# Kernel tuning notes

Hardware: AMD Instinct MI355X
Metric: run time of the kernel (lower is better)

The kernel has to match this reference:

```python
import jax, jax.numpy as jnp
import numpy as np
import math

H = 16  # n_heads


def setup_inputs() -> dict:
    key = jax.random.key(0)
    ks = jax.random.split(key, 12)
    B, S, D = 8, 1024, 1024
    inp = {
        "query": jax.random.normal(ks[0], (B, S, D), jnp.float32),
        "key_": jax.random.normal(ks[1], (B, S, D), jnp.float32),
        "value": jax.random.normal(ks[2], (B, S, D), jnp.float32),
        "mask": jnp.ones((B, S, S), jnp.int32),
        "attn_pos": jax.random.normal(ks[3], (1, H, S, S), jnp.float32),
    }
    sc = 1.0 / math.sqrt(D)
    for i, nm in enumerate(["q", "k", "v", "o"]):
        inp[f"w{nm}"] = jax.random.normal(ks[4 + i], (D, D), jnp.float32) * sc
        inp[f"b{nm}"] = jax.random.normal(ks[8 + i], (D,), jnp.float32) * 0.01
    return inp


def reference(query, key_, value, mask, attn_pos, wq, bq, wk, bk, wv, bv, wo, bo):
    B, S, D = query.shape
    dk = D // H

    def proj(x, w, b):  # [B,S,D] -> [B,H,S,dk]
        return (x @ w.T + b).reshape(B, S, H, dk).transpose(0, 2, 1, 3)

    q = proj(query, wq, bq)
    k = proj(key_, wk, bk)
    v = proj(value, wv, bv)

    # attn_pos branch: scale by sqrt(2*d_k), add positional bias
    scores = jnp.einsum("bhqd,bhkd->bhqk", q, k) / math.sqrt(2 * dk) + attn_pos
    scores = jnp.where(mask[:, None] == 0, -1e9, scores)
    p = jax.nn.softmax(scores, axis=-1)  # dropout inactive (eval)
    x = jnp.einsum("bhqk,bhkd->bhqd", p, v)
    x = x.transpose(0, 2, 1, 3).reshape(B, S, D)
    x = x @ wo.T + bo          # linears[-1] applied once...
    return x @ wo.T + bo       # ...and again, faithful to source
```

## Files before the change

### kernel.cpp

```cpp
#include <hip/hip_runtime.h>
#include <hip/hip_bf16.h>

typedef unsigned short u16;
typedef unsigned int u32;
typedef __attribute__((ext_vector_type(8))) short bfrag;
typedef __attribute__((ext_vector_type(4))) float f32x4;

#define DEVINL __device__ __forceinline__

DEVINL u16 f2bf(float f) {
  u32 u = __float_as_uint(f);
  u32 r = (u + 0x7fffu + ((u >> 16) & 1u)) >> 16;
  return (u16)r;
}
DEVINL float bf2f(u16 u) { return __uint_as_float(((u32)u) << 16); }
DEVINL u32 cvtpk(float lo, float hi) {
  u32 r;
  asm("v_cvt_pk_bf16_f32 %0, %1, %2" : "=v"(r) : "v"(lo), "v"(hi));
  return r;
}
DEVINL u16 f2bf_hw(float v) { return (u16)cvtpk(v, v); }
DEVINL float fmax3(float a, float b, float c) { return fmaxf(fmaxf(a, b), c); }

DEVINL void gload_lds16(const void* g, void* l) {
  __builtin_amdgcn_global_load_lds(
      (const __attribute__((address_space(1))) void*)g,
      (__attribute__((address_space(3))) void*)l, 16, 0, 0);
}

DEVINL void storeC(u16* C, size_t idx, float v) { C[idx] = f2bf_hw(v); }
DEVINL void storeC(float* C, size_t idx, float v) { C[idx] = v; }

#define SBAR0 __builtin_amdgcn_sched_barrier(0)

DEVINL void gemm_decode(int gid, int& m0, int& n0) {
  const int m = ((gid >> 6) << 3) | (gid & 7);
  const int n = (gid >> 3) & 7;
  m0 = m * 128;
  n0 = n * 128;
}


__global__ void prep_all(const float* __restrict__ wq, const float* __restrict__ wk,
                         const float* __restrict__ wv, const float* __restrict__ wo,
                         u16* __restrict__ o0, u16* __restrict__ o1,
                         u16* __restrict__ o2, u16* __restrict__ o3,
                         const int* __restrict__ mask, u32* __restrict__ bits,
                         u16* __restrict__ wot, const float* __restrict__ bo,
                         float* __restrict__ bo2) {
  __shared__ u16 tile[64][65];
  const int b = blockIdx.x;
  const int t = threadIdx.x;

  if (b < 4096) {
    const int which = b >> 10;
    const int i = (b & 1023) * 256 + t;
    const float* in = which == 0 ? wq : which == 1 ? wk : which == 2 ? wv : wo;
    u16* out = which == 0 ? o0 : which == 1 ? o1 : which == 2 ? o2 : o3;
    const float4 f = ((const float4*)in)[i];
    uint2 r;
    r.x = cvtpk(f.x, f.y);
    r.y = cvtpk(f.z, f.w);
    ((uint2*)out)[i] = r;
  } else if (b < 5120) {
    const size_t wi = (size_t)(b - 4096) * 256 + t;
    const int* src = mask + wi * 32;
    u32 v = 0;
#pragma unroll
    for (int i = 0; i < 8; ++i) {
      const int4 m4 = ((const int4*)src)[i];
      if (m4.x) v |= 1u << (i * 4 + 0);
      if (m4.y) v |= 1u << (i * 4 + 1);
      if (m4.z) v |= 1u << (i * 4 + 2);
      if (m4.w) v |= 1u << (i * 4 + 3);
    }
    bits[wi] = v;
  } else if (b < 5376) {
    const int bb = b - 5120;
    const int bx = bb & 15, by = bb >> 4;
#pragma unroll
    for (int p = 0; p < 4; ++p) {
      const int r = (t >> 4) + p * 16;
      const int c = (t & 15) * 4;
      const float4 f = *(const float4*)&wo[(size_t)(by * 64 + r) * 1024 + bx * 64 + c];
      tile[c + 0][r] = f2bf(f.x);
      tile[c + 1][r] = f2bf(f.y);
      tile[c + 2][r] = f2bf(f.z);
      tile[c + 3][r] = f2bf(f.w);
    }
    __syncthreads();
#pragma unroll
    for (int p = 0; p < 4; ++p) {
      const int r = (t >> 4) + p * 16;
      const int c = (t & 15) * 4;
      uint2 v;
      v.x = (u32)tile[r][c] | ((u32)tile[r][c + 1] << 16);
      v.y = (u32)tile[r][c + 2] | ((u32)tile[r][c + 3] << 16);
      *(uint2*)&wot[(size_t)(bx * 64 + r) * 1024 + by * 64 + c] = v;
    }
  } else {
    const int w = t >> 6, lane = t & 63;
    const int row = (b - 5376) * 4 + w;
    const float* src = wo + (size_t)row * 1024;
    float s = 0.f;
#pragma unroll
    for (int i = 0; i < 4; ++i) {
      const float4 f = *(const float4*)&src[lane * 4 + i * 256];
      const float4 g = *(const float4*)&bo[lane * 4 + i * 256];
      s += f.x * g.x + f.y * g.y + f.z * g.z + f.w * g.w;
    }
#pragma unroll
    for (int d = 1; d < 64; d <<= 1) s += __shfl_xor(s, d);
    if (lane == 0) bo2[row] = s + bo[row];
  }
}

__global__ __launch_bounds__(256) void gemm_bt_64(
    const u16* __restrict__ A, const u16* __restrict__ W,
    u16* __restrict__ C, int N, int K) {
  __shared__ u16 sA[64 * 64];
  __shared__ u16 sB[64 * 64];
  const int t = threadIdx.x;
  const int w = t >> 6, lane = t & 63;
  const int lr = lane & 15, lk = (lane >> 4) * 8;
  const int m0 = blockIdx.x * 64, n0 = blockIdx.y * 64;
  f32x4 acc[4] = {};
  for (int k0 = 0; k0 < K; k0 += 64) {
#pragma unroll
    for (int i = 0; i < 2; ++i) {
      const int idx = i * 256 + t;
      const int row = idx >> 3;
      const int col = (idx & 7) * 8;
      gload_lds16(A + (size_t)(m0 + row) * K + k0 + col, &sA[idx * 8]);
      gload_lds16(W + (size_t)(n0 + row) * K + k0 + col, &sB[idx * 8]);
    }
    __syncthreads();
#pragma unroll
    for (int ks = 0; ks < 2; ++ks) {
      const bfrag av = *(const bfrag*)&sA[(w * 16 + lr) * 64 + ks * 32 + lk];
#pragma unroll
      for (int n = 0; n < 4; ++n) {
        const bfrag bv = *(const bfrag*)&sB[(n * 16 + lr) * 64 + ks * 32 + lk];
        acc[n] = __builtin_amdgcn_mfma_f32_16x16x32_bf16(av, bv, acc[n], 0, 0, 0);
      }
    }
    __syncthreads();
  }
  const int orow = (lane >> 4) * 4;
#pragma unroll
  for (int n = 0; n < 4; ++n)
#pragma unroll
    for (int j = 0; j < 4; ++j)
      C[(size_t)(m0 + w * 16 + orow + j) * N + n0 + n * 16 + lr] = f2bf_hw(acc[n][j]);
}


__global__ __launch_bounds__(256) void gemm_qkv(
    const float* __restrict__ Aq, const float* __restrict__ Ak, const float* __restrict__ Av,
    const u16* __restrict__ Wq, const u16* __restrict__ Wk, const u16* __restrict__ Wv,
    const float* __restrict__ Bq, const float* __restrict__ Bk, const float* __restrict__ Bv,
    u16* __restrict__ Qb, u16* __restrict__ Kb, u16* __restrict__ Vt, float qs) {
  __shared__ __align__(16) u16 sA[128 * 64];
  __shared__ __align__(16) u16 sB[128 * 64];
  const int gid = blockIdx.x;
  const int which = gid >> 9;
  int m0, n0;
  gemm_decode(gid & 511, m0, n0);
  const float* A = which == 0 ? Aq : which == 1 ? Ak : Av;
  const u16* W = which == 0 ? Wq : which == 1 ? Wk : Wv;
  const float* bias = which == 0 ? Bq : which == 1 ? Bk : Bv;
  const int t = threadIdx.x;
  const int w = t >> 6, lane = t & 63;
  const int lr = lane & 15, lg = lane >> 4;
  const int wr = (w >> 1) * 64, wc = (w & 1) * 64;
  f32x4 acc[4][4] = {};

  for (int kt = 0; kt < 16; ++kt) {
    const int k0 = kt * 64;
    f32x4 fa[4][2];
#pragma unroll
    for (int i = 0; i < 4; ++i) {
      const int idx = i * 256 + t;
      const int row = idx >> 3;
      const int cg = idx & 7;
      const float* src = A + (size_t)(m0 + row) * 1024 + k0 + cg * 8;
      fa[i][0] = *(const f32x4*)src;
      fa[i][1] = *(const f32x4*)(src + 4);
    }
    if (kt) __syncthreads();
#pragma unroll
    for (int i = 0; i < 4; ++i) {
      const int idx = i * 256 + t;
      const int row = idx >> 3;
      const int cg = idx & 7;
      uint4 pk;
      pk.x = cvtpk(fa[i][0][0], fa[i][0][1]);
      pk.y = cvtpk(fa[i][0][2], fa[i][0][3]);
      pk.z = cvtpk(fa[i][1][0], fa[i][1][1]);
      pk.w = cvtpk(fa[i][1][2], fa[i][1][3]);
      *(uint4*)((char*)sA + row * 128 + ((cg ^ (row & 7)) * 16)) = pk;
      gload_lds16(W + (size_t)(n0 + row) * 1024 + k0 + ((cg ^ (row & 7)) * 8),
                  (char*)sB + idx * 16);
    }
    __syncthreads();
#pragma unroll
    for (int ks = 0; ks < 2; ++ks) {
      bfrag av[4], bv[4];
#pragma unroll
      for (int m = 0; m < 4; ++m) {
        const int row = wr + m * 16 + lr;
        av[m] = *(const bfrag*)((const char*)sA + row * 128 + ((ks * 64 + lg * 16) ^ ((row & 7) << 4)));
      }
#pragma unroll
      for (int n = 0; n < 4; ++n) {
        const int row = wc + n * 16 + lr;
        bv[n] = *(const bfrag*)((const char*)sB + row * 128 + ((ks * 64 + lg * 16) ^ ((row & 7) << 4)));
      }
#pragma unroll
      for (int m = 0; m < 4; ++m)
#pragma unroll
        for (int n = 0; n < 4; ++n)
          acc[m][n] = __builtin_amdgcn_mfma_f32_16x16x32_bf16(av[m], bv[n], acc[m][n], 0, 0, 0);
    }
  }

  float bz[4];
#pragma unroll
  for (int n = 0; n < 4; ++n) bz[n] = bias[n0 + wc + n * 16 + lr];
  const int orow = lg * 4;
  if (which == 2) {
#pragma unroll
    for (int m = 0; m < 4; ++m) {
#pragma unroll
      for (int n = 0; n < 4; ++n) {
        const int r0 = m0 + wr + m * 16 + orow;
        const int c = n0 + wc + n * 16 + lr;
        const int bb = r0 >> 10, s = r0 & 1023;
        const int h = c >> 6, d = c & 63;
        uint2 v;
        v.x = cvtpk(acc[m][n][0] + bz[n], acc[m][n][1] + bz[n]);
        v.y = cvtpk(acc[m][n][2] + bz[n], acc[m][n][3] + bz[n]);
        *(uint2*)&Vt[(((size_t)bb * 16 + h) * 64 + d) * 1024 + s] = v;
      }
    }
  } else {
    u16* C = which == 0 ? Qb : Kb;
    const float osc = which == 0 ? qs : 1.0f;
#pragma unroll
    for (int m = 0; m < 4; ++m) {
#pragma unroll
      for (int n = 0; n < 4; ++n) {
        const int r = m0 + wr + m * 16 + orow;
        const int c = n0 + wc + n * 16 + lr;
#pragma unroll
        for (int j = 0; j < 4; ++j)
          C[(size_t)(r + j) * 1024 + c] = f2bf_hw((acc[m][n][j] + bz[n]) * osc);
      }
    }
  }
}


template <typename OutT>
__global__ __launch_bounds__(256) void gemm_bt_a16(
    const u16* __restrict__ A, const u16* __restrict__ W,
    const float* __restrict__ bias, OutT* __restrict__ C,
    int M, int N, int K) {
  __shared__ __align__(16) u16 sA[2][128 * 64];
  __shared__ __align__(16) u16 sB[2][128 * 64];
  const int t = threadIdx.x;
  const int w = t >> 6, lane = t & 63;
  const int lr = lane & 15, lg = lane >> 4;
  int m0, n0;
  gemm_decode(blockIdx.x, m0, n0);
  const int wr = (w >> 1) * 64, wc = (w & 1) * 64;
  f32x4 acc[4][4] = {};
  const int nk = K >> 6;

#pragma unroll
  for (int i = 0; i < 4; ++i) {
    const int idx = i * 256 + t;
    const int row = idx >> 3;
    const int col = ((idx & 7) ^ (row & 7)) * 8;
    gload_lds16(A + (size_t)(m0 + row) * K + col, (char*)sA[0] + idx * 16);
    gload_lds16(W + (size_t)(n0 + row) * K + col, (char*)sB[0] + idx * 16);
  }
  SBAR0; asm volatile("s_waitcnt vmcnt(0)" ::: "memory"); SBAR0;
  __builtin_amdgcn_s_barrier(); SBAR0;

#pragma unroll 2
  for (int kt = 0; kt < nk; ++kt) {
    const int cur = kt & 1;
    if (kt < nk - 1) {
      const int k0 = (kt + 1) * 64;
#pragma unroll
      for (int i = 0; i < 4; ++i) {
        const int idx = i * 256 + t;
        const int row = idx >> 3;
        const int col = ((idx & 7) ^ (row & 7)) * 8;
        gload_lds16(A + (size_t)(m0 + row) * K + k0 + col, (char*)sA[cur ^ 1] + idx * 16);
        gload_lds16(W + (size_t)(n0 + row) * K + k0 + col, (char*)sB[cur ^ 1] + idx * 16);
      }
    }
    const char* pA = (const char*)sA[cur];
    const char* pB = (const char*)sB[cur];
#pragma unroll
    for (int ks = 0; ks < 2; ++ks) {
      bfrag av[4], bv[4];
#pragma unroll
      for (int m = 0; m < 4; ++m) {
        const int row = wr + m * 16 + lr;
        av[m] = *(const bfrag*)(pA + row * 128 + ((ks * 64 + lg * 16) ^ ((row & 7) << 4)));
      }
#pragma unroll
      for (int n = 0; n < 4; ++n) {
        const int row = wc + n * 16 + lr;
        bv[n] = *(const bfrag*)(pB + row * 128 + ((ks * 64 + lg * 16) ^ ((row & 7) << 4)));
      }
#pragma unroll
      for (int m = 0; m < 4; ++m)
#pragma unroll
        for (int n = 0; n < 4; ++n)
          acc[m][n] = __builtin_amdgcn_mfma_f32_16x16x32_bf16(av[m], bv[n], acc[m][n], 0, 0, 0);
    }
    if (kt < nk - 1) {
      SBAR0; asm volatile("s_waitcnt vmcnt(0)" ::: "memory"); SBAR0;
      __builtin_amdgcn_s_barrier(); SBAR0;
    }
  }

  float bz[4];
#pragma unroll
  for (int n = 0; n < 4; ++n) bz[n] = bias[n0 + wc + n * 16 + lr];
  const int orow = lg * 4;
#pragma unroll
  for (int m = 0; m < 4; ++m) {
#pragma unroll
    for (int n = 0; n < 4; ++n) {
      const int r = m0 + wr + m * 16 + orow;
      const int c = n0 + wc + n * 16 + lr;
#pragma unroll
      for (int j = 0; j < 4; ++j)
        storeC(C, (size_t)(r + j) * N + c, acc[m][n][j] + bz[n]);
    }
  }
}


__global__ __launch_bounds__(512, 4) void attn_fwd(
    const u16* __restrict__ Qm, const u16* __restrict__ Km,
    const u16* __restrict__ Vt, const float* __restrict__ pos,
    const u32* __restrict__ mbits, u16* __restrict__ Om) {
  const int gid = blockIdx.x;
  const int h = (gid & 7) + 8 * (gid >> 9);
  const int inner = (gid >> 3) & 63;
  const int bb = inner & 7;
  const int qt = inner >> 3;
  const int t = threadIdx.x;
  const int w = t >> 6, lane = t & 63;
  const int lr = lane & 15, lg = lane >> 4;
  const float log2e = 1.4426950408889634f;

  __shared__ __align__(16) char smem[49152];

  const int q0 = qt * 128;
  const size_t baseQ = ((size_t)bb * 1024) * 1024 + (size_t)h * 64;
  const size_t baseV = ((size_t)(bb * 16 + h) * 64) * 1024;
  const int qg = q0 + w * 16 + lr;
  const float* posrow = pos + ((size_t)h * 1024 + qg) * 1024;
  const u32* mrow = mbits + ((size_t)bb * 1024 + qg) * 32;

#pragma unroll
  for (int i = 0; i < 2; ++i) {
    const int idx = i * 512 + t;
    const int r = idx >> 3;
    const int w8 = idx & 7;
    gload_lds16(Qm + baseQ + (size_t)(q0 + r) * 1024 + (w8 ^ (r & 7)) * 8, smem + idx * 16);
  }
  {
    const int r = t >> 3;
    const int w8 = t & 7;
    gload_lds16(Km + baseQ + (size_t)r * 1024 + (w8 ^ (r & 7)) * 8, smem + 16384 + t * 16);
    gload_lds16(Vt + baseV + (size_t)r * 1024 + (w8 ^ (r & 7)) * 8, smem + 24576 + t * 16);
  }

  u32 ok = 0xffffffffu;
#pragma unroll
  for (int i = 0; i < 8; ++i) {
    const uint4 m4 = *(const uint4*)&mrow[i * 4];
    ok &= m4.x & m4.y & m4.z & m4.w;
  }
  const bool allone = __all(ok == 0xffffffffu);

  float4 pz[4];
#pragma unroll
  for (int n = 0; n < 4; ++n) pz[n] = *(const float4*)&posrow[n * 16 + lg * 4];

  __syncthreads();

  bfrag qv[2];
#pragma unroll
  for (int ks = 0; ks < 2; ++ks) {
    const int byt = (w * 16 + lr) * 128 + ((ks * 64 + lg * 16) ^ ((lr & 7) << 4));
    qv[ks] = *(const bfrag*)(smem + byt);
  }
  __syncthreads();

  f32x4 o[4] = {};
  float m_q = -3.0e38f, l_q = 0.f;

  for (int kt = 0; kt < 16; ++kt) {
    const int cur = kt & 1;
    const char* sK = smem + (cur ? 0 : 16384);
    const char* sV = smem + (cur ? 8192 : 24576);

    float4 pzn[4];
    if (kt < 15) {
      const int kn = (kt + 1) * 64;
      char* dK = smem + (cur ? 16384 : 0);
      char* dV = smem + (cur ? 24576 : 8192);
      const int r = t >> 3;
      const int w8 = t & 7;
      gload_lds16(Km + baseQ + (size_t)(kn + r) * 1024 + (w8 ^ (r & 7)) * 8, dK + t * 16);
      gload_lds16(Vt + baseV + (size_t)r * 1024 + kn + (w8 ^ (r & 7)) * 8, dV + t * 16);
#pragma unroll
      for (int n = 0; n < 4; ++n) pzn[n] = *(const float4*)&posrow[kn + n * 16 + lg * 4];
    }

    f32x4 s[4] = {};
    __builtin_amdgcn_s_setprio(1);
#pragma unroll
    for (int ks = 0; ks < 2; ++ks) {
#pragma unroll
      for (int n = 0; n < 4; ++n) {
        const int byt = (n * 16 + lr) * 128 + ((ks * 64 + lg * 16) ^ ((lr & 7) << 4));
        const bfrag kf = *(const bfrag*)(sK + byt);
        s[n] = __builtin_amdgcn_mfma_f32_16x16x32_bf16(kf, qv[ks], s[n], 0, 0, 0);
      }
    }
    __builtin_amdgcn_s_setprio(0);

    float pv[16];
#pragma unroll
    for (int n = 0; n < 4; ++n) {
      pv[n * 4 + 0] = fmaf(pz[n].x, log2e, s[n][0]);
      pv[n * 4 + 1] = fmaf(pz[n].y, log2e, s[n][1]);
      pv[n * 4 + 2] = fmaf(pz[n].z, log2e, s[n][2]);
      pv[n * 4 + 3] = fmaf(pz[n].w, log2e, s[n][3]);
    }

    if (!allone) {
      const u32 a0 = mrow[kt * 2], a1 = mrow[kt * 2 + 1];
#pragma unroll
      for (int n = 0; n < 4; ++n)
#pragma unroll
        for (int j = 0; j < 4; ++j) {
          const int kl = n * 16 + lg * 4 + j;
          const u32 mw = (kl & 32) ? a1 : a0;
          if (!((mw >> (kl & 31)) & 1u)) pv[n * 4 + j] = -1.0e9f;
        }
    }

    float tmax = fmax3(pv[0], pv[1], pv[2]);
    tmax = fmax3(tmax, pv[3], pv[4]);
    tmax = fmax3(tmax, pv[5], pv[6]);
    tmax = fmax3(tmax, pv[7], pv[8]);
    tmax = fmax3(tmax, pv[9], pv[10]);
    tmax = fmax3(tmax, pv[11], pv[12]);
    tmax = fmax3(tmax, pv[13], pv[14]);
    tmax = fmaxf(tmax, pv[15]);
    tmax = fmaxf(tmax, __shfl_xor(tmax, 16));
    tmax = fmaxf(tmax, __shfl_xor(tmax, 32));

    if (!__all(tmax <= m_q + 8.0f)) {
      const float mn = fmaxf(m_q, tmax);
      const float sc = __builtin_amdgcn_exp2f(m_q - mn);
      l_q *= sc;
#pragma unroll
      for (int j = 0; j < 4; ++j) {
        const float scj = __shfl(sc, lg * 4 + j);
#pragma unroll
        for (int n = 0; n < 4; ++n) o[n][j] *= scj;
      }
      m_q = mn;
    }
    float rs = 0.f;
#pragma unroll
    for (int i2 = 0; i2 < 16; ++i2) {
      pv[i2] = __builtin_amdgcn_exp2f(pv[i2] - m_q);
      rs += pv[i2];
    }
    rs += __shfl_xor(rs, 16);
    rs += __shfl_xor(rs, 32);
    l_q += rs;

    char* pbuf = smem + 32768 + w * 2048;
#pragma unroll
    for (int n = 0; n < 4; ++n) {
      uint2 pk;
      pk.x = cvtpk(pv[n * 4 + 0], pv[n * 4 + 1]);
      pk.y = cvtpk(pv[n * 4 + 2], pv[n * 4 + 3]);
      const int byt = lr * 128 + ((n * 32 + lg * 8) ^ ((lr & 7) << 4));
      *(uint2*)(pbuf + byt) = pk;
    }
    __builtin_amdgcn_s_setprio(1);
#pragma unroll
    for (int ks = 0; ks < 2; ++ks) {
      const int pbyt = lr * 128 + ((ks * 64 + lg * 16) ^ ((lr & 7) << 4));
      const bfrag pf = *(const bfrag*)(pbuf + pbyt);
#pragma unroll
      for (int n = 0; n < 4; ++n) {
        const int vb = (n * 16 + lr) * 128 + ((ks * 64 + lg * 16) ^ ((lr & 7) << 4));
        const bfrag vf = *(const bfrag*)(sV + vb);
        o[n] = __builtin_amdgcn_mfma_f32_16x16x32_bf16(pf, vf, o[n], 0, 0, 0);
      }
    }
    __builtin_amdgcn_s_setprio(0);

    __syncthreads();

    if (kt < 15) {
#pragma unroll
      for (int n = 0; n < 4; ++n) pz[n] = pzn[n];
    }
  }

#pragma unroll
  for (int j = 0; j < 4; ++j) {
    const float lj = __shfl(l_q, lg * 4 + j);
    const float inv = 1.f / lj;
    const int qr = q0 + w * 16 + lg * 4 + j;
#pragma unroll
    for (int n = 0; n < 4; ++n)
      Om[baseQ + (size_t)qr * 1024 + n * 16 + lr] = f2bf_hw(o[n][j] * inv);
  }
}


extern "C" void kernel_launch(void* const* d_in, const int* in_sizes, int n_in,
                              void* d_out, int out_size, void* d_ws, size_t ws_size,
                              hipStream_t stream) {
  const float* query = (const float*)d_in[0];
  const float* key_  = (const float*)d_in[1];
  const float* value = (const float*)d_in[2];
  const int*   mask  = (const int*)d_in[3];
  const float* pos   = (const float*)d_in[4];
  const float* wq = (const float*)d_in[5];
  const float* bq = (const float*)d_in[6];
  const float* wk = (const float*)d_in[7];
  const float* bk = (const float*)d_in[8];
  const float* wv = (const float*)d_in[9];
  const float* bv = (const float*)d_in[10];
  const float* wo = (const float*)d_in[11];
  const float* bo = (const float*)d_in[12];

  char* ws = (char*)d_ws;
  const size_t MB = 1024 * 1024;
  u16* wqb  = (u16*)(ws + 0 * MB);
  u16* wkb  = (u16*)(ws + 2 * MB);
  u16* wvb  = (u16*)(ws + 4 * MB);
  u16* wob  = (u16*)(ws + 6 * MB);
  u16* Qb   = (u16*)(ws + 40 * MB);
  u16* Kb   = (u16*)(ws + 56 * MB);
  u16* Vtb  = (u16*)(ws + 72 * MB);
  u16* Xa   = (u16*)(ws + 88 * MB);
  u32* mb   = (u32*)(ws + 104 * MB);
  u16* wotb = (u16*)(ws + 105 * MB);
  u16* W2b  = (u16*)(ws + 107 * MB);
  float* bo2 = (float*)(ws + 109 * MB);

  const float log2e = 1.4426950408889634f;
  const float qs = 0.0883883476483184f * log2e;

  prep_all<<<5632, 256, 0, stream>>>(wq, wk, wv, wo, wqb, wkb, wvb, wob,
                                     mask, mb, wotb, bo, bo2);

  gemm_bt_64<<<dim3(16, 16), 256, 0, stream>>>(wob, wotb, W2b, 1024, 1024);

  gemm_qkv<<<1536, 256, 0, stream>>>(query, key_, value, wqb, wkb, wvb,
                                     bq, bk, bv, Qb, Kb, Vtb, qs);

  attn_fwd<<<1024, 512, 0, stream>>>(Qb, Kb, Vtb, pos, mb, Xa);

  gemm_bt_a16<float><<<512, 256, 0, stream>>>(Xa, W2b, bo2, (float*)d_out, 8192, 1024, 1024);
}
```

Before: 225.4 us.

## Pre-convert QKV activations to bf16 and double-buffer QKV GEMM via async LDS loads

Adds a bf16 conversion pass for query/key/value to the prep kernel, so the QKV projection GEMM can read bf16 activations through direct global-to-LDS loads instead of loading fp32 and converting in registers. The GEMM main loop is rewritten with double-buffered LDS tiles that prefetch the next k-tile while MFMAs run on the current one. This trades an extra pass over the activations (one fp32 read plus a bf16 write and re-read) for a lighter, overlapped inner loop. LDS use doubles, and Vin shares workspace with Xa, which is only safe because attention writes Xa after the GEMM finishes.

```diff
diff --git a/kernel.cpp b/kernel.cpp
--- a/kernel.cpp
+++ b/kernel.cpp
@@ -47,7 +47,11 @@
                          u16* __restrict__ o2, u16* __restrict__ o3,
                          const int* __restrict__ mask, u32* __restrict__ bits,
                          u16* __restrict__ wot, const float* __restrict__ bo,
-                         float* __restrict__ bo2) {
+                         float* __restrict__ bo2,
+                         const float* __restrict__ qf, const float* __restrict__ kf,
+                         const float* __restrict__ vf,
+                         u16* __restrict__ qo, u16* __restrict__ ko,
+                         u16* __restrict__ vo) {
   __shared__ u16 tile[64][65];
   const int b = blockIdx.x;
   const int t = threadIdx.x;
@@ -98,7 +102,7 @@
       v.y = (u32)tile[r][c + 2] | ((u32)tile[r][c + 3] << 16);
       *(uint2*)&wot[(size_t)(bx * 64 + r) * 1024 + by * 64 + c] = v;
     }
-  } else {
+  } else if (b < 5632) {
     const int w = t >> 6, lane = t & 63;
     const int row = (b - 5376) * 4 + w;
     const float* src = wo + (size_t)row * 1024;
@@ -112,6 +116,20 @@
 #pragma unroll
     for (int d = 1; d < 64; d <<= 1) s += __shfl_xor(s, d);
     if (lane == 0) bo2[row] = s + bo[row];
+  } else {
+    const int bb2 = b - 5632;
+    const int which = bb2 >> 12;
+    const size_t base = ((size_t)(bb2 & 4095) * 256 + t) * 8;
+    const float* in = which == 0 ? qf : which == 1 ? kf : vf;
+    u16* out = which == 0 ? qo : which == 1 ? ko : vo;
+    const f32x4 f0 = *(const f32x4*)(in + base);
+    const f32x4 f1 = *(const f32x4*)(in + base + 4);
+    uint4 r;
+    r.x = cvtpk(f0[0], f0[1]);
+    r.y = cvtpk(f0[2], f0[3]);
+    r.z = cvtpk(f1[0], f1[1]);
+    r.w = cvtpk(f1[2], f1[3]);
+    *(uint4*)(out + base) = r;
   }
 }
 
@@ -155,18 +173,18 @@
 }
 
 
-__global__ __launch_bounds__(256) void gemm_qkv(
-    const float* __restrict__ Aq, const float* __restrict__ Ak, const float* __restrict__ Av,
+__global__ __launch_bounds__(256) void gemm_qkv_a16(
+    const u16* __restrict__ Aq, const u16* __restrict__ Ak, const u16* __restrict__ Av,
     const u16* __restrict__ Wq, const u16* __restrict__ Wk, const u16* __restrict__ Wv,
     const float* __restrict__ Bq, const float* __restrict__ Bk, const float* __restrict__ Bv,
     u16* __restrict__ Qb, u16* __restrict__ Kb, u16* __restrict__ Vt, float qs) {
-  __shared__ __align__(16) u16 sA[128 * 64];
-  __shared__ __align__(16) u16 sB[128 * 64];
+  __shared__ __align__(16) u16 sA[2][128 * 64];
+  __shared__ __align__(16) u16 sB[2][128 * 64];
   const int gid = blockIdx.x;
   const int which = gid >> 9;
   int m0, n0;
   gemm_decode(gid & 511, m0, n0);
-  const float* A = which == 0 ? Aq : which == 1 ? Ak : Av;
+  const u16* A = which == 0 ? Aq : which == 1 ? Ak : Av;
   const u16* W = which == 0 ? Wq : which == 1 ? Wk : Wv;
   const float* bias = which == 0 ? Bq : which == 1 ? Bk : Bv;
   const int t = threadIdx.x;
@@ -174,53 +192,57 @@
   const int lr = lane & 15, lg = lane >> 4;
   const int wr = (w >> 1) * 64, wc = (w & 1) * 64;
   f32x4 acc[4][4] = {};
-
-  for (int kt = 0; kt < 16; ++kt) {
-    const int k0 = kt * 64;
-    f32x4 fa[4][2];
-#pragma unroll
-    for (int i = 0; i < 4; ++i) {
-      const int idx = i * 256 + t;
-      const int row = idx >> 3;
-      const int cg = idx & 7;
-      const float* src = A + (size_t)(m0 + row) * 1024 + k0 + cg * 8;
-      fa[i][0] = *(const f32x4*)src;
-      fa[i][1] = *(const f32x4*)(src + 4);
-    }
-    if (kt) __syncthreads();
-#pragma unroll
-    for (int i = 0; i < 4; ++i) {
-      const int idx = i * 256 + t;
-      const int row = idx >> 3;
-      const int cg = idx & 7;
-      uint4 pk;
-      pk.x = cvtpk(fa[i][0][0], fa[i][0][1]);
-      pk.y = cvtpk(fa[i][0][2], fa[i][0][3]);
-      pk.z = cvtpk(fa[i][1][0], fa[i][1][1]);
-      pk.w = cvtpk(fa[i][1][2], fa[i][1][3]);
-      *(uint4*)((char*)sA + row * 128 + ((cg ^ (row & 7)) * 16)) = pk;
-      gload_lds16(W + (size_t)(n0 + row) * 1024 + k0 + ((cg ^ (row & 7)) * 8),
-                  (char*)sB + idx * 16);
-    }
-    __syncthreads();
+  const int nk = 16;
+
+#pragma unroll
+  for (int i = 0; i < 4; ++i) {
+    const int idx = i * 256 + t;
+    const int row = idx >> 3;
+    const int col = ((idx & 7) ^ (row & 7)) * 8;
+    gload_lds16(A + (size_t)(m0 + row) * 1024 + col, (char*)sA[0] + idx * 16);
+    gload_lds16(W + (size_t)(n0 + row) * 1024 + col, (char*)sB[0] + idx * 16);
+  }
+  SBAR0; asm volatile("s_waitcnt vmcnt(0)" ::: "memory"); SBAR0;
+  __builtin_amdgcn_s_barrier(); SBAR0;
+
+#pragma unroll 2
+  for (int kt = 0; kt < nk; ++kt) {
+    const int cur = kt & 1;
+    if (kt < nk - 1) {
+      const int k0 = (kt + 1) * 64;
+#pragma unroll
+      for (int i = 0; i < 4; ++i) {
+        const int idx = i * 256 + t;
+        const int row = idx >> 3;
+        const int col = ((idx & 7) ^ (row & 7)) * 8;
+        gload_lds16(A + (size_t)(m0 + row) * 1024 + k0 + col, (char*)sA[cur ^ 1] + idx * 16);
+        gload_lds16(W + (size_t)(n0 + row) * 1024 + k0 + col, (char*)sB[cur ^ 1] + idx * 16);
+      }
+    }
+    const char* pA = (const char*)sA[cur];
+    const char* pB = (const char*)sB[cur];
 #pragma unroll
     for (int ks = 0; ks < 2; ++ks) {
       bfrag av[4], bv[4];
 #pragma unroll
       for (int m = 0; m < 4; ++m) {
         const int row = wr + m * 16 + lr;
-        av[m] = *(const bfrag*)((const char*)sA + row * 128 + ((ks * 64 + lg * 16) ^ ((row & 7) << 4)));
+        av[m] = *(const bfrag*)(pA + row * 128 + ((ks * 64 + lg * 16) ^ ((row & 7) << 4)));
       }
 #pragma unroll
       for (int n = 0; n < 4; ++n) {
         const int row = wc + n * 16 + lr;
-        bv[n] = *(const bfrag*)((const char*)sB + row * 128 + ((ks * 64 + lg * 16) ^ ((row & 7) << 4)));
+        bv[n] = *(const bfrag*)(pB + row * 128 + ((ks * 64 + lg * 16) ^ ((row & 7) << 4)));
       }
 #pragma unroll
       for (int m = 0; m < 4; ++m)
 #pragma unroll
         for (int n = 0; n < 4; ++n)
           acc[m][n] = __builtin_amdgcn_mfma_f32_16x16x32_bf16(av[m], bv[n], acc[m][n], 0, 0, 0);
+    }
+    if (kt < nk - 1) {
+      SBAR0; asm volatile("s_waitcnt vmcnt(0)" ::: "memory"); SBAR0;
+      __builtin_amdgcn_s_barrier(); SBAR0;
     }
   }
 
@@ -560,10 +582,13 @@
   u16* wkb  = (u16*)(ws + 2 * MB);
   u16* wvb  = (u16*)(ws + 4 * MB);
   u16* wob  = (u16*)(ws + 6 * MB);
+  u16* Qin  = (u16*)(ws + 8 * MB);
+  u16* Kin  = (u16*)(ws + 24 * MB);
   u16* Qb   = (u16*)(ws + 40 * MB);
   u16* Kb   = (u16*)(ws + 56 * MB);
   u16* Vtb  = (u16*)(ws + 72 * MB);
   u16* Xa   = (u16*)(ws + 88 * MB);
+  u16* Vin  = (u16*)(ws + 88 * MB);
   u32* mb   = (u32*)(ws + 104 * MB);
   u16* wotb = (u16*)(ws + 105 * MB);
   u16* W2b  = (u16*)(ws + 107 * MB);
@@ -572,13 +597,14 @@
   const float log2e = 1.4426950408889634f;
   const float qs = 0.0883883476483184f * log2e;
 
-  prep_all<<<5632, 256, 0, stream>>>(wq, wk, wv, wo, wqb, wkb, wvb, wob,
-                                     mask, mb, wotb, bo, bo2);
+  prep_all<<<17920, 256, 0, stream>>>(wq, wk, wv, wo, wqb, wkb, wvb, wob,
+                                      mask, mb, wotb, bo, bo2,
+                                      query, key_, value, Qin, Kin, Vin);
 
   gemm_bt_64<<<dim3(16, 16), 256, 0, stream>>>(wob, wotb, W2b, 1024, 1024);
 
-  gemm_qkv<<<1536, 256, 0, stream>>>(query, key_, value, wqb, wkb, wvb,
-                                     bq, bk, bv, Qb, Kb, Vtb, qs);
+  gemm_qkv_a16<<<1536, 256, 0, stream>>>(Qin, Kin, Vin, wqb, wkb, wvb,
+                                         bq, bk, bv, Qb, Kb, Vtb, qs);
 
   attn_fwd<<<1024, 512, 0, stream>>>(Qb, Kb, Vtb, pos, mb, Xa);
 
```

Result: no change. 228.8 us (+1.5%).
